# Kernel optimization log

Hardware: AMD Instinct MI355X
Metric: run time of the kernel (lower is better)

Reference implementation:

```python
import jax, jax.numpy as jnp
import numpy as np

# dims
B, N, D, E, TOPK = 8, 16384, 256, 8, 2
HID = D // 2
ROUTING_FLOOR = min(0.05, 0.15 / 4)  # min(base, 0.15/num_experts_B)


def setup_inputs() -> dict:
    key = jax.random.key(0)
    ks = jax.random.split(key, 8)
    tokens = jax.random.normal(ks[0], (B, N, D), dtype=jnp.float32)
    spatial_xyz = jax.random.normal(ks[1], (B, N, 3), dtype=jnp.float32) * 10.0
    t = jax.random.randint(ks[2], (B,), 0, 1000, dtype=jnp.int32)
    # gate_proj: Linear(D+3 -> D//2) -> GELU -> Linear(D//2 -> E)
    W1 = jax.random.normal(ks[3], (D + 3, HID), dtype=jnp.float32) * 0.02
    b1 = jnp.zeros((HID,), dtype=jnp.float32)
    W2 = jax.random.normal(ks[4], (HID, E), dtype=jnp.float32) * 0.02
    b2 = jnp.zeros((E,), dtype=jnp.float32)
    # expert spatial centers: randn(E,3) * 10
    centers = jax.random.normal(ks[5], (E, 3), dtype=jnp.float32) * 10.0
    return {
        "tokens": tokens,
        "spatial_xyz": spatial_xyz,
        "W1": W1,
        "b1": b1,
        "W2": W2,
        "b2": b2,
        "centers": centers,
        "t": t,
    }


def reference(tokens, spatial_xyz, W1, b1, W2, b2, centers, t):
    # tokens: (B,N,D)  spatial_xyz: (B,N,3)  centers: (E,3)
    Bv, Nv, Dv = tokens.shape
    Ev = centers.shape[0]
    # pairwise euclidean distances, (B,N,E)  (== torch.cdist)
    diff = spatial_xyz[:, :, None, :] - centers[None, None, :, :]
    dists = jnp.sqrt(jnp.sum(diff * diff, axis=-1))
    spatial_affinity = -dists / (dists.mean() + 1e-6)
    # content gate MLP
    gate_input = jnp.concatenate([tokens, spatial_xyz], axis=-1)  # (B,N,D+3)
    h = jax.nn.gelu(gate_input @ W1 + b1, approximate=False)
    content_logits = h @ W2 + b2  # (B,N,E)
    logits = content_logits + spatial_affinity
    # expert-choice routing: each expert picks its top tokens
    expert_logits = jnp.swapaxes(logits, 1, 2)  # (B,E,N)
    tokens_per_expert = max(1, Nv * TOPK // Ev)
    k = min(tokens_per_expert, Nv)
    topk_vals, topk_idx = jax.lax.top_k(expert_logits, k)  # (B,E,k)
    dispatch = jnp.zeros((Bv, Ev, Nv), dtype=tokens.dtype)
    dispatch = dispatch.at[
        jnp.arange(Bv)[:, None, None],
        jnp.arange(Ev)[None, :, None],
        topk_idx,
    ].set(jax.nn.sigmoid(topk_vals))
    dispatch = jnp.swapaxes(dispatch, 1, 2)  # (B,N,E)
    # routing floor: interpolate toward uniform
    alpha = min(ROUTING_FLOOR * Ev, 1.0)
    return (1.0 - alpha) * dispatch + alpha / Ev
```

## Files before the change

kernel.cpp:

```cpp
#include <hip/hip_runtime.h>
#include <hip/hip_bf16.h>
#include <math.h>

#define Bq   8
#define Nq   16384
#define Dq   256
#define Eq   8
#define HIDq 128
#define KSEL 4096
#define TOKENS (Bq * Nq)

#define SCALEq 0.7f
#define FLOORq 0.0375f

#define CONT_OFF 0u
#define DIST_OFF 4194304u
#define SUM_OFF  8388608u
#define TAU_OFF  (8388608u + 256u)
#define CUT_OFF  (8388608u + 512u)

#define TOK_BLK 64
#define KT      32

__device__ __forceinline__ unsigned key_of(float f) {
    unsigned u = __float_as_uint(f);
    return (u & 0x80000000u) ? ~u : (u | 0x80000000u);
}

__global__ __launch_bounds__(256, 4) void kA(
    const float* __restrict__ tokens, const float* __restrict__ xyz,
    const float* __restrict__ W1, const float* __restrict__ b1,
    const float* __restrict__ W2, const float* __restrict__ b2,
    const float* __restrict__ centers,
    float* __restrict__ content, float* __restrict__ dvals,
    double* __restrict__ sumd)
{
    __shared__ float ltok[TOK_BLK][KT + 4];
    __shared__ float w1s[KT][HIDq + 4];
    __shared__ float sW2[HIDq * Eq];
    __shared__ float sxyz[TOK_BLK * 3];
    __shared__ float pw[4][TOK_BLK][Eq + 1];

    const int t    = threadIdx.x;
    const int w    = t >> 6;
    const int jg   = t >> 4;
    const int tg   = t & 15;
    const int base = blockIdx.x * TOK_BLK;

    *reinterpret_cast<float4*>(&sW2[t * 4]) =
        *reinterpret_cast<const float4*>(W2 + t * 4);
    if (t < TOK_BLK * 3) sxyz[t] = xyz[(size_t)base * 3 + t];

    if (t < TOK_BLK) {
        const int token = base + t;
        const int bb = token >> 14, nn = token & (Nq - 1);
        const float x0 = xyz[(size_t)token * 3 + 0];
        const float x1 = xyz[(size_t)token * 3 + 1];
        const float x2 = xyz[(size_t)token * 3 + 2];
        double local = 0.0;
        #pragma unroll
        for (int e = 0; e < Eq; ++e) {
            float dx = x0 - centers[e * 3 + 0];
            float dy = x1 - centers[e * 3 + 1];
            float dz = x2 - centers[e * 3 + 2];
            float s  = (dx * dx + dy * dy) + dz * dz;
            float dd = sqrtf(s);
            dvals[((size_t)bb * Eq + e) * Nq + nn] = dd;
            local += (double)dd;
        }
        #pragma unroll
        for (int off = 32; off > 0; off >>= 1)
            local += __shfl_down(local, off);
        if (t == 0) atomicAdd(sumd, local);
    }

    float acc[4][8];
    #pragma unroll
    for (int jj = 0; jj < 8; ++jj) {
        const float bv = b1[jg * 8 + jj];
        #pragma unroll
        for (int i = 0; i < 4; ++i) acc[i][jj] = bv;
    }

    for (int kt = 0; kt < Dq / KT; ++kt) {
        __syncthreads();
        #pragma unroll
        for (int p = 0; p < 2; ++p) {
            const int f = p * 256 + t;
            const int row = f >> 3, col = f & 7;
            const float4 v = *reinterpret_cast<const float4*>(
                tokens + (size_t)(base + row) * Dq + kt * KT + col * 4);
            float2* dst = reinterpret_cast<float2*>(&ltok[row][col * 4]);
            dst[0] = make_float2(v.x, v.y);
            dst[1] = make_float2(v.z, v.w);
        }
        #pragma unroll
        for (int q = 0; q < 4; ++q) {
            const int f = q * 256 + t;
            const int kr = f >> 5, col = f & 31;
            *reinterpret_cast<float4*>(&w1s[kr][col * 4]) =
                *reinterpret_cast<const float4*>(
                    W1 + (size_t)(kt * KT + kr) * HIDq + col * 4);
        }
        __syncthreads();
        #pragma unroll 4
        for (int k = 0; k < KT; ++k) {
            const float a0 = ltok[tg][k];
            const float a1 = ltok[tg + 16][k];
            const float a2 = ltok[tg + 32][k];
            const float a3 = ltok[tg + 48][k];
            const float4 wv0 = *reinterpret_cast<const float4*>(&w1s[k][jg * 8]);
            const float4 wv1 = *reinterpret_cast<const float4*>(&w1s[k][jg * 8 + 4]);
            const float wj[8] = {wv0.x, wv0.y, wv0.z, wv0.w,
                                 wv1.x, wv1.y, wv1.z, wv1.w};
            #pragma unroll
            for (int jj = 0; jj < 8; ++jj) {
                acc[0][jj] = fmaf(a0, wj[jj], acc[0][jj]);
                acc[1][jj] = fmaf(a1, wj[jj], acc[1][jj]);
                acc[2][jj] = fmaf(a2, wj[jj], acc[2][jj]);
                acc[3][jj] = fmaf(a3, wj[jj], acc[3][jj]);
            }
        }
    }

    {
        float xr[3][4];
        #pragma unroll
        for (int i = 0; i < 4; ++i) {
            xr[0][i] = sxyz[(tg + 16 * i) * 3 + 0];
            xr[1][i] = sxyz[(tg + 16 * i) * 3 + 1];
            xr[2][i] = sxyz[(tg + 16 * i) * 3 + 2];
        }
        #pragma unroll
        for (int c = 0; c < 3; ++c) {
            float wrow[8];
            #pragma unroll
            for (int jj = 0; jj < 8; ++jj)
                wrow[jj] = W1[(size_t)(Dq + c) * HIDq + jg * 8 + jj];
            #pragma unroll
            for (int jj = 0; jj < 8; ++jj) {
                acc[0][jj] = fmaf(xr[c][0], wrow[jj], acc[0][jj]);
                acc[1][jj] = fmaf(xr[c][1], wrow[jj], acc[1][jj]);
                acc[2][jj] = fmaf(xr[c][2], wrow[jj], acc[2][jj]);
                acc[3][jj] = fmaf(xr[c][3], wrow[jj], acc[3][jj]);
            }
        }
    }

    float pe[4][8];
    #pragma unroll
    for (int i = 0; i < 4; ++i)
        #pragma unroll
        for (int e = 0; e < Eq; ++e) pe[i][e] = 0.0f;
    #pragma unroll
    for (int jj = 0; jj < 8; ++jj) {
        float w2r[8];
        #pragma unroll
        for (int e = 0; e < Eq; ++e) w2r[e] = sW2[(jg * 8 + jj) * Eq + e];
        #pragma unroll
        for (int i = 0; i < 4; ++i) {
            const float v = acc[i][jj];
            const float g = 0.5f * v * (1.0f + erff(v * 0.70710678118654752440f));
            #pragma unroll
            for (int e = 0; e < Eq; ++e)
                pe[i][e] = fmaf(g, w2r[e], pe[i][e]);
        }
    }

    #pragma unroll
    for (int i = 0; i < 4; ++i)
        #pragma unroll
        for (int e = 0; e < Eq; ++e) {
            float x = pe[i][e];
            x += __shfl_xor(x, 16);
            x += __shfl_xor(x, 32);
            pe[i][e] = x;
        }
    if ((t & 48) == 0) {
        #pragma unroll
        for (int i = 0; i < 4; ++i)
            #pragma unroll
            for (int e = 0; e < Eq; ++e)
                pw[w][tg + 16 * i][e] = pe[i][e];
    }
    __syncthreads();

    #pragma unroll
    for (int s = 0; s < 2; ++s) {
        const int id = s * 256 + t;
        const int e  = id >> 6;
        const int tl = id & 63;
        const int token = base + tl;
        const int bb = token >> 14, nn = token & (Nq - 1);
        float tot = b2[e] + pw[0][tl][e] + pw[1][tl][e]
                          + pw[2][tl][e] + pw[3][tl][e];
        content[((size_t)bb * Eq + e) * Nq + nn] = tot;
    }
}

__global__ __launch_bounds__(1024, 1) void kB(
    const float* __restrict__ content, const float* __restrict__ dvals,
    const double* __restrict__ sumd,
    unsigned* __restrict__ tau_out, int* __restrict__ cut_out)
{
    const int be = blockIdx.x;
    const int t  = threadIdx.x;

    __shared__ unsigned hist[256];
    __shared__ unsigned sufa[256];
    __shared__ unsigned sc[2];
    __shared__ unsigned mcnt[1024];

    const float meanf = (float)(sumd[0] * (1.0 / (double)(Bq * Nq * Eq)));
    const float denom = meanf + 1e-6f;

    const float* __restrict__ ce = content + (size_t)be * Nq;
    const float* __restrict__ de = dvals   + (size_t)be * Nq;

    unsigned prefix = 0, mask = 0;
    int needed = KSEL;
    for (int pass = 0; pass < 4; ++pass) {
        const int shift = 24 - 8 * pass;
        if (t < 256) hist[t] = 0;
        __syncthreads();
        for (int i = t; i < Nq; i += 1024) {
            float aff = (-de[i]) / denom;
            float lg  = ce[i] + aff;
            unsigned kk = key_of(lg);
            if ((kk & mask) == prefix)
                atomicAdd(&hist[(kk >> shift) & 0xFFu], 1u);
        }
        __syncthreads();
        if (t < 256) sufa[t] = hist[t];
        __syncthreads();
        for (int st = 1; st < 256; st <<= 1) {
            unsigned v = 0, a = 0;
            if (t < 256) {
                v = sufa[t];
                a = (t + st < 256) ? sufa[t + st] : 0u;
            }
            __syncthreads();
            if (t < 256) sufa[t] = v + a;
            __syncthreads();
        }
        if (t < 256) {
            unsigned mine = sufa[t];
            unsigned hi   = (t < 255) ? sufa[t + 1] : 0u;
            if (mine >= (unsigned)needed && hi < (unsigned)needed) {
                sc[0] = (unsigned)t;
                sc[1] = (unsigned)needed - hi;
            }
        }
        __syncthreads();
        prefix |= sc[0] << shift;
        mask   |= 0xFFu << shift;
        needed  = (int)sc[1];
        __syncthreads();
    }

    const int bi = t * 16;
    int mym = 0;
    for (int i = 0; i < 16; ++i) {
        float aff = (-de[bi + i]) / denom;
        float lg  = ce[bi + i] + aff;
        mym += (key_of(lg) == prefix);
    }
    mcnt[t] = (unsigned)mym;
    __syncthreads();
    for (int st = 1; st < 1024; st <<= 1) {
        unsigned v = mcnt[t];
        unsigned a = (t >= st) ? mcnt[t - st] : 0u;
        __syncthreads();
        mcnt[t] = v + a;
        __syncthreads();
    }
    const int incl = (int)mcnt[t];
    const int excl = incl - mym;
    if (excl < needed && incl >= needed) {
        int r2 = needed - excl, c = 0, cut = bi;
        for (int i = 0; i < 16; ++i) {
            float aff = (-de[bi + i]) / denom;
            float lg  = ce[bi + i] + aff;
            if (key_of(lg) == prefix) {
                if (++c == r2) { cut = bi + i; break; }
            }
        }
        tau_out[be] = prefix;
        cut_out[be] = cut;
    }
}

__global__ __launch_bounds__(256) void kC(
    const float* __restrict__ content, const float* __restrict__ dvals,
    const double* __restrict__ sumd,
    const unsigned* __restrict__ tau, const int* __restrict__ cut,
    float* __restrict__ out)
{
    const int idx = blockIdx.x * 256 + threadIdx.x;
    const int b = idx >> 14;
    const int n = idx & (Nq - 1);

    const float meanf = (float)(sumd[0] * (1.0 / (double)(Bq * Nq * Eq)));
    const float denom = meanf + 1e-6f;

    #pragma unroll
    for (int e = 0; e < Eq; ++e) {
        const size_t bt = ((size_t)b * Eq + e) * Nq + n;
        float aff = (-dvals[bt]) / denom;
        float lg  = content[bt] + aff;
        unsigned k  = key_of(lg);
        unsigned tk = tau[b * Eq + e];
        bool sel = (k > tk) || (k == tk && n <= cut[b * Eq + e]);
        float disp = sel ? (1.0f / (1.0f + expf(-lg))) : 0.0f;
        out[(size_t)idx * Eq + e] = fmaf(SCALEq, disp, FLOORq);
    }
}

extern "C" void kernel_launch(void* const* d_in, const int* in_sizes, int n_in,
                              void* d_out, int out_size, void* d_ws, size_t ws_size,
                              hipStream_t stream) {
    const float* tokens  = (const float*)d_in[0];
    const float* xyz     = (const float*)d_in[1];
    const float* W1      = (const float*)d_in[2];
    const float* b1      = (const float*)d_in[3];
    const float* W2      = (const float*)d_in[4];
    const float* b2      = (const float*)d_in[5];
    const float* centers = (const float*)d_in[6];

    char* ws = (char*)d_ws;
    float*    content = (float*)(ws + CONT_OFF);
    float*    dvals   = (float*)(ws + DIST_OFF);
    double*   sumd    = (double*)(ws + SUM_OFF);
    unsigned* tau     = (unsigned*)(ws + TAU_OFF);
    int*      cutv    = (int*)(ws + CUT_OFF);

    hipMemsetAsync(sumd, 0, sizeof(double), stream);
    kA<<<TOKENS / TOK_BLK, 256, 0, stream>>>(tokens, xyz, W1, b1, W2, b2,
                                             centers, content, dvals, sumd);
    kB<<<Bq * Eq, 1024, 0, stream>>>(content, dvals, sumd, tau, cutv);
    kC<<<TOKENS / 256, 256, 0, stream>>>(content, dvals, sumd, tau, cutv,
                                         (float*)d_out);
}
```

Baseline: 344.5 us.

## Prefetch GEMM tiles in registers, cache radix keys, and use wave-level scans

In the gate MLP kernel, the next K-tile of tokens and W1 is loaded into registers while the current tile is being computed, so global latency overlaps the FMA loop. The token tile and the partial-sum buffer now share one shared-memory region, which needs an extra barrier. In the top-k selection kernel, each thread computes its 16 logit keys once and keeps them in registers for all radix passes, instead of re-reading content and distance values every pass. The block-wide shared-memory suffix and prefix scans are replaced with wave shuffle scans, cutting the number of barriers at the cost of more register pressure.

After: 322.7 us. 1.07x faster.

```diff
diff --git a/kernel.cpp b/kernel.cpp
--- a/kernel.cpp
+++ b/kernel.cpp
@@ -35,17 +35,36 @@
     float* __restrict__ content, float* __restrict__ dvals,
     double* __restrict__ sumd)
 {
-    __shared__ float ltok[TOK_BLK][KT + 4];
     __shared__ float w1s[KT][HIDq + 4];
+    __shared__ __align__(16) float uni[TOK_BLK * (KT + 4)];
     __shared__ float sW2[HIDq * Eq];
     __shared__ float sxyz[TOK_BLK * 3];
-    __shared__ float pw[4][TOK_BLK][Eq + 1];
+
+    float (*ltok)[KT + 4] = reinterpret_cast<float (*)[KT + 4]>(uni);
+    float (*pw)[TOK_BLK][Eq + 1] =
+        reinterpret_cast<float (*)[TOK_BLK][Eq + 1]>(uni);
 
     const int t    = threadIdx.x;
     const int w    = t >> 6;
     const int jg   = t >> 4;
     const int tg   = t & 15;
     const int base = blockIdx.x * TOK_BLK;
+
+    const int trow = t >> 3, tcol = t & 7;
+    const int wrow = t >> 5, wcol = t & 31;
+
+    float4 t0 = *reinterpret_cast<const float4*>(
+        tokens + (size_t)(base + trow) * Dq + tcol * 4);
+    float4 t1 = *reinterpret_cast<const float4*>(
+        tokens + (size_t)(base + 32 + trow) * Dq + tcol * 4);
+    float4 w0 = *reinterpret_cast<const float4*>(
+        W1 + (size_t)(wrow) * HIDq + wcol * 4);
+    float4 w1v = *reinterpret_cast<const float4*>(
+        W1 + (size_t)(8 + wrow) * HIDq + wcol * 4);
+    float4 w2v = *reinterpret_cast<const float4*>(
+        W1 + (size_t)(16 + wrow) * HIDq + wcol * 4);
+    float4 w3v = *reinterpret_cast<const float4*>(
+        W1 + (size_t)(24 + wrow) * HIDq + wcol * 4);
 
     *reinterpret_cast<float4*>(&sW2[t * 4]) =
         *reinterpret_cast<const float4*>(W2 + t * 4);
@@ -84,25 +103,28 @@
 
     for (int kt = 0; kt < Dq / KT; ++kt) {
         __syncthreads();
-        #pragma unroll
-        for (int p = 0; p < 2; ++p) {
-            const int f = p * 256 + t;
-            const int row = f >> 3, col = f & 7;
-            const float4 v = *reinterpret_cast<const float4*>(
-                tokens + (size_t)(base + row) * Dq + kt * KT + col * 4);
-            float2* dst = reinterpret_cast<float2*>(&ltok[row][col * 4]);
-            dst[0] = make_float2(v.x, v.y);
-            dst[1] = make_float2(v.z, v.w);
-        }
-        #pragma unroll
-        for (int q = 0; q < 4; ++q) {
-            const int f = q * 256 + t;
-            const int kr = f >> 5, col = f & 31;
-            *reinterpret_cast<float4*>(&w1s[kr][col * 4]) =
-                *reinterpret_cast<const float4*>(
-                    W1 + (size_t)(kt * KT + kr) * HIDq + col * 4);
-        }
-        __syncthreads();
+        *reinterpret_cast<float4*>(&ltok[trow][tcol * 4])      = t0;
+        *reinterpret_cast<float4*>(&ltok[32 + trow][tcol * 4]) = t1;
+        *reinterpret_cast<float4*>(&w1s[wrow][wcol * 4])       = w0;
+        *reinterpret_cast<float4*>(&w1s[8 + wrow][wcol * 4])   = w1v;
+        *reinterpret_cast<float4*>(&w1s[16 + wrow][wcol * 4])  = w2v;
+        *reinterpret_cast<float4*>(&w1s[24 + wrow][wcol * 4])  = w3v;
+        __syncthreads();
+        if (kt < Dq / KT - 1) {
+            const int k0 = (kt + 1) * KT;
+            t0 = *reinterpret_cast<const float4*>(
+                tokens + (size_t)(base + trow) * Dq + k0 + tcol * 4);
+            t1 = *reinterpret_cast<const float4*>(
+                tokens + (size_t)(base + 32 + trow) * Dq + k0 + tcol * 4);
+            w0 = *reinterpret_cast<const float4*>(
+                W1 + (size_t)(k0 + wrow) * HIDq + wcol * 4);
+            w1v = *reinterpret_cast<const float4*>(
+                W1 + (size_t)(k0 + 8 + wrow) * HIDq + wcol * 4);
+            w2v = *reinterpret_cast<const float4*>(
+                W1 + (size_t)(k0 + 16 + wrow) * HIDq + wcol * 4);
+            w3v = *reinterpret_cast<const float4*>(
+                W1 + (size_t)(k0 + 24 + wrow) * HIDq + wcol * 4);
+        }
         #pragma unroll 4
         for (int k = 0; k < KT; ++k) {
             const float a0 = ltok[tg][k];
@@ -133,16 +155,16 @@
         }
         #pragma unroll
         for (int c = 0; c < 3; ++c) {
-            float wrow[8];
+            float wrow8[8];
             #pragma unroll
             for (int jj = 0; jj < 8; ++jj)
-                wrow[jj] = W1[(size_t)(Dq + c) * HIDq + jg * 8 + jj];
+                wrow8[jj] = W1[(size_t)(Dq + c) * HIDq + jg * 8 + jj];
             #pragma unroll
             for (int jj = 0; jj < 8; ++jj) {
-                acc[0][jj] = fmaf(xr[c][0], wrow[jj], acc[0][jj]);
-                acc[1][jj] = fmaf(xr[c][1], wrow[jj], acc[1][jj]);
-                acc[2][jj] = fmaf(xr[c][2], wrow[jj], acc[2][jj]);
-                acc[3][jj] = fmaf(xr[c][3], wrow[jj], acc[3][jj]);
+                acc[0][jj] = fmaf(xr[c][0], wrow8[jj], acc[0][jj]);
+                acc[1][jj] = fmaf(xr[c][1], wrow8[jj], acc[1][jj]);
+                acc[2][jj] = fmaf(xr[c][2], wrow8[jj], acc[2][jj]);
+                acc[3][jj] = fmaf(xr[c][3], wrow8[jj], acc[3][jj]);
             }
         }
     }
@@ -176,6 +198,8 @@
             x += __shfl_xor(x, 32);
             pe[i][e] = x;
         }
+
+    __syncthreads();
     if ((t & 48) == 0) {
         #pragma unroll
         for (int i = 0; i < 4; ++i)
@@ -203,13 +227,13 @@
     const double* __restrict__ sumd,
     unsigned* __restrict__ tau_out, int* __restrict__ cut_out)
 {
-    const int be = blockIdx.x;
-    const int t  = threadIdx.x;
+    const int be   = blockIdx.x;
+    const int t    = threadIdx.x;
+    const int lane = t & 63, wv = t >> 6;
 
     __shared__ unsigned hist[256];
-    __shared__ unsigned sufa[256];
     __shared__ unsigned sc[2];
-    __shared__ unsigned mcnt[1024];
+    __shared__ unsigned wsum[16];
 
     const float meanf = (float)(sumd[0] * (1.0 / (double)(Bq * Nq * Eq)));
     const float denom = meanf + 1e-6f;
@@ -217,39 +241,52 @@
     const float* __restrict__ ce = content + (size_t)be * Nq;
     const float* __restrict__ de = dvals   + (size_t)be * Nq;
 
+    const int i0 = t * 16;
+    unsigned key[16];
+    #pragma unroll
+    for (int q = 0; q < 4; ++q) {
+        const float4 c4 = *reinterpret_cast<const float4*>(ce + i0 + q * 4);
+        const float4 d4 = *reinterpret_cast<const float4*>(de + i0 + q * 4);
+        key[q * 4 + 0] = key_of(c4.x + (-d4.x) / denom);
+        key[q * 4 + 1] = key_of(c4.y + (-d4.y) / denom);
+        key[q * 4 + 2] = key_of(c4.z + (-d4.z) / denom);
+        key[q * 4 + 3] = key_of(c4.w + (-d4.w) / denom);
+    }
+
     unsigned prefix = 0, mask = 0;
     int needed = KSEL;
+    #pragma unroll
     for (int pass = 0; pass < 4; ++pass) {
         const int shift = 24 - 8 * pass;
         if (t < 256) hist[t] = 0;
         __syncthreads();
-        for (int i = t; i < Nq; i += 1024) {
-            float aff = (-de[i]) / denom;
-            float lg  = ce[i] + aff;
-            unsigned kk = key_of(lg);
-            if ((kk & mask) == prefix)
-                atomicAdd(&hist[(kk >> shift) & 0xFFu], 1u);
-        }
-        __syncthreads();
-        if (t < 256) sufa[t] = hist[t];
-        __syncthreads();
-        for (int st = 1; st < 256; st <<= 1) {
-            unsigned v = 0, a = 0;
-            if (t < 256) {
-                v = sufa[t];
-                a = (t + st < 256) ? sufa[t + st] : 0u;
+        #pragma unroll
+        for (int j = 0; j < 16; ++j)
+            if ((key[j] & mask) == prefix)
+                atomicAdd(&hist[(key[j] >> shift) & 0xFFu], 1u);
+        __syncthreads();
+        if (wv == 0) {
+            const unsigned h0 = hist[4 * lane + 0];
+            const unsigned h1 = hist[4 * lane + 1];
+            const unsigned h2 = hist[4 * lane + 2];
+            const unsigned h3 = hist[4 * lane + 3];
+            const unsigned s3 = h3, s2 = h2 + s3, s1 = h1 + s2, s0 = h0 + s1;
+            unsigned tot = s0;
+            #pragma unroll
+            for (int off = 1; off < 64; off <<= 1) {
+                unsigned u = __shfl_down(tot, off);
+                if (lane + off < 64) tot += u;
             }
-            __syncthreads();
-            if (t < 256) sufa[t] = v + a;
-            __syncthreads();
-        }
-        if (t < 256) {
-            unsigned mine = sufa[t];
-            unsigned hi   = (t < 255) ? sufa[t + 1] : 0u;
-            if (mine >= (unsigned)needed && hi < (unsigned)needed) {
-                sc[0] = (unsigned)t;
-                sc[1] = (unsigned)needed - hi;
-            }
+            unsigned totN = __shfl_down(tot, 1);
+            if (lane == 63) totN = 0;
+            const unsigned beyond = tot - s0;
+            const unsigned sufa0 = s0 + beyond, sufa1 = s1 + beyond,
+                           sufa2 = s2 + beyond, sufa3 = s3 + beyond;
+            const unsigned nd = (unsigned)needed;
+            if (sufa0 >= nd && sufa1 < nd) { sc[0] = 4u*lane + 0; sc[1] = nd - sufa1; }
+            if (sufa1 >= nd && sufa2 < nd) { sc[0] = 4u*lane + 1; sc[1] = nd - sufa2; }
+            if (sufa2 >= nd && sufa3 < nd) { sc[0] = 4u*lane + 2; sc[1] = nd - sufa3; }
+            if (sufa3 >= nd && totN  < nd) { sc[0] = 4u*lane + 3; sc[1] = nd - totN;  }
         }
         __syncthreads();
         prefix |= sc[0] << shift;
@@ -258,31 +295,27 @@
         __syncthreads();
     }
 
-    const int bi = t * 16;
     int mym = 0;
-    for (int i = 0; i < 16; ++i) {
-        float aff = (-de[bi + i]) / denom;
-        float lg  = ce[bi + i] + aff;
-        mym += (key_of(lg) == prefix);
-    }
-    mcnt[t] = (unsigned)mym;
+    #pragma unroll
+    for (int j = 0; j < 16; ++j) mym += (key[j] == prefix);
+    unsigned v = (unsigned)mym;
+    #pragma unroll
+    for (int off = 1; off < 64; off <<= 1) {
+        unsigned u = __shfl_up(v, off);
+        if (lane >= off) v += u;
+    }
+    if (lane == 63) wsum[wv] = v;
     __syncthreads();
-    for (int st = 1; st < 1024; st <<= 1) {
-        unsigned v = mcnt[t];
-        unsigned a = (t >= st) ? mcnt[t - st] : 0u;
-        __syncthreads();
-        mcnt[t] = v + a;
-        __syncthreads();
-    }
-    const int incl = (int)mcnt[t];
+    unsigned woff = 0;
+    for (int q2 = 0; q2 < wv; ++q2) woff += wsum[q2];
+    const int incl = (int)(woff + v);
     const int excl = incl - mym;
     if (excl < needed && incl >= needed) {
-        int r2 = needed - excl, c = 0, cut = bi;
-        for (int i = 0; i < 16; ++i) {
-            float aff = (-de[bi + i]) / denom;
-            float lg  = ce[bi + i] + aff;
-            if (key_of(lg) == prefix) {
-                if (++c == r2) { cut = bi + i; break; }
+        int r2 = needed - excl, c = 0, cut = i0;
+        #pragma unroll
+        for (int j = 0; j < 16; ++j) {
+            if (key[j] == prefix) {
+                if (++c == r2) { cut = i0 + j; }
             }
         }
         tau_out[be] = prefix;
```
